# Optimization experiments

Measured on AMD Instinct MI355X. Metric: run time of the kernel, lower is better.

The kernel has to match this reference:

```python
import jax, jax.numpy as jnp
import numpy as np
from jax import lax


def conv1x1(x, w, b):
    # x: [B,C,H,W], w: [O,C], b: [O]
    return jnp.einsum('bchw,oc->bohw', x, w) + b[None, :, None, None]


def dwconv3(x, w, b):
    # depthwise 3x3, SAME padding. x: [B,C,H,W], w: [C,1,3,3], b: [C]
    C = x.shape[1]
    y = lax.conv_general_dilated(x, w, (1, 1), 'SAME',
                                 dimension_numbers=('NCHW', 'OIHW', 'NCHW'),
                                 feature_group_count=C)
    return y + b[None, :, None, None]


def proj(x, w1, b1, wd, bd):
    return dwconv3(conv1x1(x, w1, b1), wd, bd)


def setup_inputs() -> dict:
    key = jax.random.key(0)
    B, C, H, W = 8, 96, 256, 256
    ks = jax.random.split(key, 32)
    s = 0.05

    def rn(k, shape, scale=s):
        return jax.random.normal(k, shape, dtype=jnp.float32) * scale

    inp = {
        'I1': jax.random.normal(ks[0], (B, H * W, C), dtype=jnp.float32),
        'I2': jax.random.normal(ks[1], (B, H * W, C), dtype=jnp.float32),
        'h': H, 'w': W,
        'se1_w': rn(ks[2], (C, C)), 'se1_b': rn(ks[3], (C,)),
        'se1_dw': rn(ks[4], (C, 1, 3, 3)), 'se1_db': rn(ks[5], (C,)),
        'se2_w': rn(ks[6], (C, C)), 'se2_b': rn(ks[7], (C,)),
        'se2_dw': rn(ks[8], (C, 1, 3, 3)), 'se2_db': rn(ks[9], (C,)),
        'lp1_w': rn(ks[10], (C, C)), 'lp1_b': rn(ks[11], (C,)),
        'lp1_dw': rn(ks[12], (C, 1, 3, 3)), 'lp1_db': rn(ks[13], (C,)),
        'rp1_w': rn(ks[14], (C, C)), 'rp1_b': rn(ks[15], (C,)),
        'rp1_dw': rn(ks[16], (C, 1, 3, 3)), 'rp1_db': rn(ks[17], (C,)),
        'lp2_w': rn(ks[18], (C, C)), 'lp2_b': rn(ks[19], (C,)),
        'rp2_w': rn(ks[20], (C, C)), 'rp2_b': rn(ks[21], (C,)),
        'down_w': rn(ks[22], (C, 2 * C)), 'down_b': rn(ks[23], (C,)),
        'beta': rn(ks[24], (1, C, 1, 1), 0.1),
        'gamma': rn(ks[25], (1, C, 1, 1), 0.1),
    }
    return inp


def reference(I1, I2, h, w, se1_w, se1_b, se1_dw, se1_db, se2_w, se2_b,
              se2_dw, se2_db, lp1_w, lp1_b, lp1_dw, lp1_db, rp1_w, rp1_b,
              rp1_dw, rp1_db, lp2_w, lp2_b, rp2_w, rp2_b, down_w, down_b,
              beta, gamma):
    B, HW, C = I1.shape
    scale = C ** (-0.5)
    # PatchUnEmbed: [B, HW, C] -> [B, C, h, w]
    x_l = jnp.transpose(I1, (0, 2, 1)).reshape(B, C, h, w)
    x_r = jnp.transpose(I2, (0, 2, 1)).reshape(B, C, h, w)

    Q_l = jnp.transpose(proj(x_l, se1_w, se1_b, se1_dw, se1_db), (0, 2, 3, 1))  # [B,H,W,C]
    Q_r = jnp.transpose(proj(x_r, se2_w, se2_b, se2_dw, se2_db), (0, 2, 3, 1))  # [B,H,W,C]
    V_l = jnp.transpose(proj(x_l, lp1_w, lp1_b, lp1_dw, lp1_db), (0, 2, 3, 1))
    V_r = jnp.transpose(proj(x_r, rp1_w, rp1_b, rp1_dw, rp1_db), (0, 2, 3, 1))

    # row-wise cross attention along width: [B,H,W,W]
    attn = jax.nn.softmax(jnp.einsum('bhwc,bhvc->bhwv', Q_l, Q_r), axis=-1) * scale
    F_r2l = jnp.einsum('bhwv,bhvc->bhwc', attn, V_r)  # [B,H,W,C]
    F_l2r = jnp.einsum('bhwv,bhwc->bhvc', attn, V_l)  # attn^T @ V_l

    F_r2l = conv1x1(jnp.transpose(F_r2l, (0, 3, 1, 2)), lp2_w, lp2_b) * beta
    F_l2r = conv1x1(jnp.transpose(F_l2r, (0, 3, 1, 2)), rp2_w, rp2_b) * gamma

    fuse = conv1x1(jnp.concatenate([x_l + F_r2l, x_r + F_l2r], axis=1), down_w, down_b)
    # [B,C,H,W] -> [B, HW, C]
    return jnp.transpose(fuse.reshape(B, C, HW), (0, 2, 1))
```

## Files before the change

### kernel.cpp

```cpp
#include <hip/hip_runtime.h>
#include <hip/hip_bf16.h>
#include <stdint.h>

typedef __bf16 bf;
typedef __bf16 bfv8 __attribute__((ext_vector_type(8)));
typedef __bf16 bfv4 __attribute__((ext_vector_type(4)));
typedef float  f32x4 __attribute__((ext_vector_type(4)));

#define MFMA16(a,b,c) __builtin_amdgcn_mfma_f32_16x16x32_bf16((a),(b),(c),0,0,0)

#define CH  96
#define WID 256
#define HGT 256
#define NB  8
#define SCALE 0.1020620726159658f

__device__ __forceinline__ float b2f(bf x){ return (float)x; }
__device__ __forceinline__ bf   f2b(float x){ return (bf)x; }

__device__ __forceinline__ bfv8 ld_cvt8(const float* __restrict__ p){
  f32x4 a = *(const f32x4*)p;
  f32x4 b = *(const f32x4*)(p + 4);
  bfv8 r;
  r[0]=f2b(a[0]); r[1]=f2b(a[1]); r[2]=f2b(a[2]); r[3]=f2b(a[3]);
  r[4]=f2b(b[0]); r[5]=f2b(b[1]); r[6]=f2b(b[2]); r[7]=f2b(b[3]);
  return r;
}
__device__ __forceinline__ bfv4 pack4(float a,float b,float c,float d){
  bfv4 r; r[0]=f2b(a); r[1]=f2b(b); r[2]=f2b(c); r[3]=f2b(d); return r;
}

__global__ __launch_bounds__(256) void k_c1x1(
    const float* __restrict__ X,
    const float* __restrict__ Wa, const float* __restrict__ Ba,
    const float* __restrict__ Wb, const float* __restrict__ Bb,
    bf* __restrict__ Ca, bf* __restrict__ Cb)
{
  const int tid=threadIdx.x, lane=tid&63, wv=tid>>6;
  const int l15=lane&15, lg=lane>>4;
  const int set = wv&1, th = wv>>1;
  const float* W1 = set ? Wb : Wa;
  const float* B1 = set ? Bb : Ba;
  bf* C = set ? Cb : Ca;
  const size_t p0 = (size_t)blockIdx.x * 256;
  const int t0 = th*8;

  bfv8 wf[6][3];
  f32x4 bias4[6];
#pragma unroll
  for (int nt=0;nt<6;++nt){
    bias4[nt] = *(const f32x4*)(B1 + nt*16 + lg*4);
#pragma unroll
    for (int ks=0;ks<3;++ks)
      wf[nt][ks] = ld_cvt8(W1 + (nt*16+l15)*CH + ks*32 + lg*8);
  }

  bfv8 af[2][3], afn[2][3];
#pragma unroll
  for (int t=0;t<2;++t)
#pragma unroll
    for (int ks=0;ks<3;++ks)
      af[t][ks] = ld_cvt8(X + (p0 + (t0+t)*16 + l15)*CH + ks*32 + lg*8);

#pragma unroll 1
  for (int p=0;p<4;++p){
    if (p<3){
#pragma unroll
      for (int t=0;t<2;++t)
#pragma unroll
        for (int ks=0;ks<3;++ks)
          afn[t][ks] = ld_cvt8(X + (p0 + (t0+p*2+2+t)*16 + l15)*CH + ks*32 + lg*8);
    }
    f32x4 acc[2][6];
#pragma unroll
    for (int t=0;t<2;++t)
#pragma unroll
      for (int nt=0;nt<6;++nt) acc[t][nt]=bias4[nt];
#pragma unroll
    for (int ks=0;ks<3;++ks)
#pragma unroll
      for (int nt=0;nt<6;++nt)
#pragma unroll
        for (int t=0;t<2;++t)
          acc[t][nt] = MFMA16(wf[nt][ks], af[t][ks], acc[t][nt]);
#pragma unroll
    for (int t=0;t<2;++t){
      const int m0 = (t0+p*2+t)*16;
#pragma unroll
      for (int nt=0;nt<6;++nt)
        *(bfv4*)(C + (p0+m0+l15)*CH + nt*16 + lg*4)
          = pack4(acc[t][nt][0],acc[t][nt][1],acc[t][nt][2],acc[t][nt][3]);
    }
#pragma unroll
    for (int t=0;t<2;++t)
#pragma unroll
      for (int ks=0;ks<3;++ks) af[t][ks]=afn[t][ks];
  }
}

__global__ __launch_bounds__(256) void k_dw(
    const bf* __restrict__ C0, const bf* __restrict__ C1,
    const float* __restrict__ WD0, const float* __restrict__ BD0,
    const float* __restrict__ WD1, const float* __restrict__ BD1,
    bf* __restrict__ O0, bf* __restrict__ O1)
{
  const int tid = threadIdx.x;
  if (tid >= 240) return;
  const int g = tid % 12, slot = tid / 12;
  const int yrow = slot >> 2, xrun = slot & 3;
  const int b = blockIdx.z >> 1, s = blockIdx.z & 1;
  const bf* C = s ? C1 : C0;
  const float* WD = s ? WD1 : WD0;
  const float* BD = s ? BD1 : BD0;
  bf* O = s ? O1 : O0;
  const int x0 = blockIdx.x*64 + xrun*16;
  const int y  = blockIdx.y*5 + yrow;
  if (y >= HGT) return;
  const size_t ib = (size_t)b * (HGT*WID) * CH;

  float wv[9][8], bb[8];
#pragma unroll
  for (int j=0;j<8;++j){
    bb[j] = BD[g*8+j];
#pragma unroll
    for (int t=0;t<9;++t) wv[t][j] = WD[(g*8+j)*9 + t];
  }

  const bf* r0 = C + ib + ((size_t)(y-1)*WID)*CH + g*8;
  const bf* r1 = C + ib + ((size_t)(y  )*WID)*CH + g*8;
  const bf* r2 = C + ib + ((size_t)(y+1)*WID)*CH + g*8;
  const bool v0 = (y > 0), v2 = (y+1 < HGT);
  const bfv8 Z = {0,0,0,0,0,0,0,0};

  bfv8 w00,w01,w02, w10,w11,w12, w20,w21,w22;
  bfv8 na0,na1,na2, nb0,nb1,nb2;
  {
    bool vx = (x0 > 0);
    size_t o = (size_t)(x0-1)*CH;
    w00 = (v0&&vx) ? *(const bfv8*)(r0+o) : Z;
    w10 = vx       ? *(const bfv8*)(r1+o) : Z;
    w20 = (v2&&vx) ? *(const bfv8*)(r2+o) : Z;
  }
  {
    size_t o = (size_t)x0*CH;
    w01 = v0 ? *(const bfv8*)(r0+o) : Z;
    w11 =      *(const bfv8*)(r1+o);
    w21 = v2 ? *(const bfv8*)(r2+o) : Z;
  }
  {
    int xn = x0+1; bool vx = (xn < WID);
    size_t o = (size_t)xn*CH;
    na0 = (v0&&vx) ? *(const bfv8*)(r0+o) : Z;
    na1 = vx       ? *(const bfv8*)(r1+o) : Z;
    na2 = (v2&&vx) ? *(const bfv8*)(r2+o) : Z;
  }
  {
    int xn = x0+2; bool vx = (xn < WID);
    size_t o = (size_t)xn*CH;
    nb0 = (v0&&vx) ? *(const bfv8*)(r0+o) : Z;
    nb1 = vx       ? *(const bfv8*)(r1+o) : Z;
    nb2 = (v2&&vx) ? *(const bfv8*)(r2+o) : Z;
  }
#pragma unroll
  for (int xi=0; xi<16; ++xi){
    w02 = na0; w12 = na1; w22 = na2;
    na0 = nb0; na1 = nb1; na2 = nb2;
    {
      int xn = x0 + xi + 3;
      bool vx = (xn < WID) && (xi < 14);
      size_t o = (size_t)xn*CH;
      nb0 = (v0&&vx) ? *(const bfv8*)(r0+o) : Z;
      nb1 = vx       ? *(const bfv8*)(r1+o) : Z;
      nb2 = (v2&&vx) ? *(const bfv8*)(r2+o) : Z;
    }
    float acc[8];
#pragma unroll
    for (int j=0;j<8;++j) acc[j] = bb[j];
#pragma unroll
    for (int j=0;j<8;++j){
      acc[j] += wv[0][j]*b2f(w00[j]);
      acc[j] += wv[1][j]*b2f(w01[j]);
      acc[j] += wv[2][j]*b2f(w02[j]);
      acc[j] += wv[3][j]*b2f(w10[j]);
      acc[j] += wv[4][j]*b2f(w11[j]);
      acc[j] += wv[5][j]*b2f(w12[j]);
      acc[j] += wv[6][j]*b2f(w20[j]);
      acc[j] += wv[7][j]*b2f(w21[j]);
      acc[j] += wv[8][j]*b2f(w22[j]);
    }
    bfv8 st;
#pragma unroll
    for (int j=0;j<8;++j) st[j] = f2b(acc[j]);
    *(bfv8*)(O + ib + ((size_t)y*WID + x0 + xi)*CH + g*8) = st;
    w00=w01; w01=w02;
    w10=w11; w11=w12;
    w20=w21; w21=w22;
  }
}

__global__ __launch_bounds__(256) void k_attn(
    const bf* __restrict__ Ql, const bf* __restrict__ Qr,
    bf* Vl, bf* Vr)
{
  extern __shared__ char sm[];
  bf* vt = (bf*)sm;
  bf* aq = (bf*)(sm + 96*264*2);
  float* rs = (float*)(sm + 96*264*2 + 4*16*104*2);
  const int tid=threadIdx.x, lane=tid&63, wid=tid>>6;
  const int l15=lane&15, lg=lane>>4;
  bf* aqw = aq + wid*(16*104);
  const int bh = blockIdx.x;
  const size_t qoff = (size_t)bh * (WID*CH);

#pragma unroll 1
  for (int phase=0; phase<2; ++phase) {
    const bf* msrc = phase ? Qr+qoff : Ql+qoff;
    const bf* nsrc = phase ? Ql+qoff : Qr+qoff;
    bf* Vp = (phase ? Vl : Vr) + qoff;
    if (phase) {
      __syncthreads();
      rs[tid] = SCALE / rs[tid];
    }
    {
      const bfv8* src = (const bfv8*)(Vp + (size_t)tid*CH);
#pragma unroll
      for (int i=0;i<12;++i){
        bfv8 v8 = src[i];
#pragma unroll
        for (int j=0;j<8;++j) vt[(i*8+j)*264 + tid] = v8[j];
      }
    }
    __syncthreads();

#pragma unroll 1
    for (int qp=0; qp<2; ++qp){
      bfv8 af2[2][3];
#pragma unroll
      for (int q01=0;q01<2;++q01){
        const int m0 = (qp*2+q01)*64 + wid*16;
#pragma unroll
        for (int ks=0;ks<3;++ks)
          af2[q01][ks] = *(const bfv8*)(msrc + (size_t)(m0+l15)*CH + ks*32 + lg*8);
      }
      f32x4 o[2][6];
#pragma unroll
      for (int q01=0;q01<2;++q01)
#pragma unroll
        for (int nt=0;nt<6;++nt) o[q01][nt]=(f32x4){0.f,0.f,0.f,0.f};
      float rsum2[2]={0.f,0.f};

#pragma unroll 1
      for (int c4=0;c4<4;++c4){
        bfv8 nb[4][3];
#pragma unroll
        for (int nt=0;nt<4;++nt)
#pragma unroll
          for (int ks=0;ks<3;++ks)
            nb[nt][ks] = *(const bfv8*)(nsrc + (size_t)(c4*64+nt*16+l15)*CH + ks*32+lg*8);
        f32x4 fwv4[4];
        if (phase){
#pragma unroll
          for (int nt=0;nt<4;++nt)
            fwv4[nt] = *(const f32x4*)(rs + c4*64 + nt*16 + lg*4);
        }
#pragma unroll
        for (int q01=0;q01<2;++q01){
          f32x4 acc[4];
#pragma unroll
          for (int nt=0;nt<4;++nt) acc[nt]=(f32x4){0.f,0.f,0.f,0.f};
#pragma unroll
          for (int ks=0;ks<3;++ks)
#pragma unroll
            for (int nt=0;nt<4;++nt)
              acc[nt]=MFMA16(nb[nt][ks], af2[q01][ks], acc[nt]);
          if (phase==0){
#pragma unroll
            for (int nt=0;nt<4;++nt){
              float e0=__expf(acc[nt][0]), e1=__expf(acc[nt][1]);
              float e2=__expf(acc[nt][2]), e3=__expf(acc[nt][3]);
              rsum2[q01] += (e0+e1)+(e2+e3);
              *(bfv4*)(aqw + l15*104 + nt*16 + lg*4) = pack4(e0,e1,e2,e3);
            }
          } else {
#pragma unroll
            for (int nt=0;nt<4;++nt){
              float e0=__expf(acc[nt][0])*fwv4[nt][0];
              float e1=__expf(acc[nt][1])*fwv4[nt][1];
              float e2=__expf(acc[nt][2])*fwv4[nt][2];
              float e3=__expf(acc[nt][3])*fwv4[nt][3];
              *(bfv4*)(aqw + l15*104 + nt*16 + lg*4) = pack4(e0,e1,e2,e3);
            }
          }
#pragma unroll
          for (int ks=0;ks<2;++ks){
            bfv8 aa = *(const bfv8*)(aqw + l15*104 + ks*32 + lg*8);
#pragma unroll
            for (int nt=0;nt<6;++nt)
              o[q01][nt]=MFMA16(
                *(const bfv8*)(vt + (nt*16+l15)*264 + c4*64 + ks*32 + lg*8),
                aa, o[q01][nt]);
          }
        }
      }
#pragma unroll
      for (int q01=0;q01<2;++q01){
        const int m0 = (qp*2+q01)*64 + wid*16;
        float sc;
        if (phase==0){
          float rsv = rsum2[q01];
          rsv += __shfl_xor(rsv, 16, 64);
          rsv += __shfl_xor(rsv, 32, 64);
          if (lane < 16) rs[m0 + l15] = rsv;
          sc = SCALE / rsv;
        } else sc = 1.f;
#pragma unroll
        for (int nt=0;nt<6;++nt)
          *(bfv4*)(aqw + l15*104 + nt*16 + lg*4)
            = pack4(o[q01][nt][0]*sc, o[q01][nt][1]*sc,
                    o[q01][nt][2]*sc, o[q01][nt][3]*sc);
        const size_t pbase = (size_t)m0;
#pragma unroll
        for (int i=0;i<3;++i){
          int u=lane+64*i; int gr=u/12, sg=u%12;
          *(bfv8*)(Vp + (pbase+gr)*CH + sg*8)
            = *(const bfv8*)(aqw + gr*104 + sg*8);
        }
      }
    }
  }
}

__global__ __launch_bounds__(256) void k_wprep(
    const float* __restrict__ L, const float* __restrict__ lb,
    const float* __restrict__ R, const float* __restrict__ rb,
    const float* __restrict__ D, const float* __restrict__ db,
    const float* __restrict__ beta, const float* __restrict__ gamma,
    bf* __restrict__ Wcat, float* __restrict__ bv)
{
  const int o = blockIdx.x;
  const int tid = threadIdx.x;
  for (int k = tid; k < 384; k += 256){
    float v;
    if (k < 192) v = D[o*192 + k];
    else if (k < 288){
      int c = k - 192; float s = 0.f;
      for (int m=0;m<96;++m) s += D[o*192+m]*beta[m]*L[m*96+c];
      v = s;
    } else {
      int c = k - 288; float s = 0.f;
      for (int m=0;m<96;++m) s += D[o*192+96+m]*gamma[m]*R[m*96+c];
      v = s;
    }
    Wcat[o*384+k] = f2b(v);
  }
  if (tid == 0){
    float s = db[o];
    for (int m=0;m<96;++m) s += D[o*192+m]*beta[m]*lb[m] + D[o*192+96+m]*gamma[m]*rb[m];
    bv[o] = s;
  }
}

__global__ __launch_bounds__(256) void k_fuse(
    const float* __restrict__ I1, const float* __restrict__ I2,
    const bf* __restrict__ F1, const bf* __restrict__ F2,
    const bf* __restrict__ Wcat, const float* __restrict__ bv,
    float* __restrict__ OUT)
{
  const int tid=threadIdx.x, lane=tid&63, wv=tid>>6;
  const int l15=lane&15, lg=lane>>4;
  const int half = wv&1, pair = wv>>1;
  const size_t p0 = (size_t)blockIdx.x * 128;

  bfv8 wf[12][3];
  f32x4 bias4[3];
#pragma unroll
  for (int j=0;j<3;++j){
    int c = (half*3+j)*16;
    bias4[j] = *(const f32x4*)(bv + c + lg*4);
#pragma unroll
    for (int kb=0;kb<12;++kb)
      wf[kb][j] = *(const bfv8*)(Wcat + (size_t)(c+l15)*384 + kb*32 + lg*8);
  }

  bfv8 a[12], an[12];
  {
    const size_t m0 = p0 + pair*4*16;
    const float* x1 = I1 + (m0+l15)*CH + lg*8;
    const float* x2 = I2 + (m0+l15)*CH + lg*8;
    const bf* f1 = F1 + (m0+l15)*CH + lg*8;
    const bf* f2 = F2 + (m0+l15)*CH + lg*8;
#pragma unroll
    for (int ks=0;ks<3;++ks){
      a[ks]   = ld_cvt8(x1 + ks*32);
      a[3+ks] = ld_cvt8(x2 + ks*32);
      a[6+ks] = *(const bfv8*)(f1 + ks*32);
      a[9+ks] = *(const bfv8*)(f2 + ks*32);
    }
  }
#pragma unroll 1
  for (int i=0;i<4;++i){
    const size_t m0 = p0 + (pair*4+i)*16;
    if (i<3){
      const size_t mn = m0 + 16;
      const float* x1 = I1 + (mn+l15)*CH + lg*8;
      const float* x2 = I2 + (mn+l15)*CH + lg*8;
      const bf* f1 = F1 + (mn+l15)*CH + lg*8;
      const bf* f2 = F2 + (mn+l15)*CH + lg*8;
#pragma unroll
      for (int ks=0;ks<3;++ks){
        an[ks]   = ld_cvt8(x1 + ks*32);
        an[3+ks] = ld_cvt8(x2 + ks*32);
        an[6+ks] = *(const bfv8*)(f1 + ks*32);
        an[9+ks] = *(const bfv8*)(f2 + ks*32);
      }
    }
    f32x4 acc[3];
#pragma unroll
    for (int j=0;j<3;++j) acc[j]=bias4[j];
#pragma unroll
    for (int kb=0;kb<12;++kb)
#pragma unroll
      for (int j=0;j<3;++j)
        acc[j] = MFMA16(wf[kb][j], a[kb], acc[j]);
#pragma unroll
    for (int j=0;j<3;++j)
      *(f32x4*)(OUT + (m0+l15)*CH + (half*3+j)*16 + lg*4) = acc[j];
#pragma unroll
    for (int kb=0;kb<12;++kb) a[kb]=an[kb];
  }
}

extern "C" void kernel_launch(void* const* d_in, const int* in_sizes, int n_in,
                              void* d_out, int out_size, void* d_ws, size_t ws_size,
                              hipStream_t stream)
{
  (void)in_sizes; (void)n_in; (void)out_size; (void)ws_size;
  const float* I1 = (const float*)d_in[0];
  const float* I2 = (const float*)d_in[1];
  const float* se1_w = (const float*)d_in[4];
  const float* se1_b = (const float*)d_in[5];
  const float* se1_dw= (const float*)d_in[6];
  const float* se1_db= (const float*)d_in[7];
  const float* se2_w = (const float*)d_in[8];
  const float* se2_b = (const float*)d_in[9];
  const float* se2_dw= (const float*)d_in[10];
  const float* se2_db= (const float*)d_in[11];
  const float* lp1_w = (const float*)d_in[12];
  const float* lp1_b = (const float*)d_in[13];
  const float* lp1_dw= (const float*)d_in[14];
  const float* lp1_db= (const float*)d_in[15];
  const float* rp1_w = (const float*)d_in[16];
  const float* rp1_b = (const float*)d_in[17];
  const float* rp1_dw= (const float*)d_in[18];
  const float* rp1_db= (const float*)d_in[19];
  const float* lp2_w = (const float*)d_in[20];
  const float* lp2_b = (const float*)d_in[21];
  const float* rp2_w = (const float*)d_in[22];
  const float* rp2_b = (const float*)d_in[23];
  const float* down_w= (const float*)d_in[24];
  const float* down_b= (const float*)d_in[25];
  const float* beta  = (const float*)d_in[26];
  const float* gamma = (const float*)d_in[27];
  float* OUT = (float*)d_out;

  const size_t FIELD = (size_t)NB * HGT * WID * CH;
  bf* Ql = (bf*)d_ws;
  bf* Qr = Ql + FIELD;
  bf* Vl = Qr + FIELD;
  bf* Vr = Vl + FIELD;
  bf* Wcat = Vr + FIELD;
  float* bv = (float*)(Wcat + 96*384);
  bf* Cq = (bf*)d_out;
  bf* Cv = Cq + FIELD;

  dim3 blk(256,1,1);
  k_wprep<<<dim3(96,1,1), blk, 0, stream>>>(lp2_w, lp2_b, rp2_w, rp2_b,
        down_w, down_b, beta, gamma, Wcat, bv);
  k_c1x1<<<dim3(2048,1,1), blk, 0, stream>>>(I1, se1_w, se1_b, lp1_w, lp1_b, Cq, Cv);
  k_dw  <<<dim3(4,52,16),  blk, 0, stream>>>(Cq, Cv, se1_dw, se1_db, lp1_dw, lp1_db, Ql, Vl);
  k_c1x1<<<dim3(2048,1,1), blk, 0, stream>>>(I2, se2_w, se2_b, rp1_w, rp1_b, Cq, Cv);
  k_dw  <<<dim3(4,52,16),  blk, 0, stream>>>(Cq, Cv, se2_dw, se2_db, rp1_dw, rp1_db, Qr, Vr);
  k_attn<<<dim3(NB*HGT,1,1), blk, 96*264*2 + 4*16*104*2 + 256*4, stream>>>(Ql, Qr, Vl, Vr);
  k_fuse<<<dim3(4096,1,1), blk, 0, stream>>>(I1, I2, Vr, Vl, Wcat, bv, OUT);
}
```

Before: 978.3 us.

## Fuse final down-projection GEMM into attention kernel epilogue

Removes the separate k_fuse launch and runs the 1x1 fuse projection at the end of k_attn, with each block processing its own image row of 256 pixels. The intent is to save a kernel launch and to read the F_r2l/F_l2r rows while they are likely still in cache. In exchange the weights are read from global memory inside the MFMA loop instead of being held in registers, and the loads are no longer software-prefetched. Register pressure in k_attn may also rise and lower occupancy.

```diff
diff --git a/kernel.cpp b/kernel.cpp
--- a/kernel.cpp
+++ b/kernel.cpp
@@ -200,7 +200,10 @@
 
 __global__ __launch_bounds__(256) void k_attn(
     const bf* __restrict__ Ql, const bf* __restrict__ Qr,
-    bf* Vl, bf* Vr)
+    bf* Vl, bf* Vr,
+    const float* __restrict__ I1, const float* __restrict__ I2,
+    const bf* __restrict__ Wcat, const float* __restrict__ bv,
+    float* __restrict__ OUT)
 {
   extern __shared__ char sm[];
   bf* vt = (bf*)sm;
@@ -327,6 +330,47 @@
         }
       }
     }
+  }
+
+  __syncthreads();
+  const float* x1b = I1 + qoff;
+  const float* x2b = I2 + qoff;
+  const bf* f1b = Vr + qoff;
+  const bf* f2b_ = Vl + qoff;
+  float* outb = OUT + qoff;
+#pragma unroll 1
+  for (int i=0;i<4;++i){
+    const int m0 = wid*64 + i*16;
+    f32x4 acc[6];
+#pragma unroll
+    for (int nt=0;nt<6;++nt) acc[nt] = *(const f32x4*)(bv + nt*16 + lg*4);
+#pragma unroll 1
+    for (int kc=0;kc<2;++kc){
+      bfv8 a[6];
+      if (kc==0){
+#pragma unroll
+        for (int ks=0;ks<3;++ks){
+          a[ks]   = ld_cvt8(x1b + (size_t)(m0+l15)*CH + ks*32 + lg*8);
+          a[3+ks] = ld_cvt8(x2b + (size_t)(m0+l15)*CH + ks*32 + lg*8);
+        }
+      } else {
+#pragma unroll
+        for (int ks=0;ks<3;++ks){
+          a[ks]   = *(const bfv8*)(f1b  + (size_t)(m0+l15)*CH + ks*32 + lg*8);
+          a[3+ks] = *(const bfv8*)(f2b_ + (size_t)(m0+l15)*CH + ks*32 + lg*8);
+        }
+      }
+#pragma unroll
+      for (int kb=0;kb<6;++kb)
+#pragma unroll
+        for (int nt=0;nt<6;++nt)
+          acc[nt] = MFMA16(
+            *(const bfv8*)(Wcat + (size_t)(nt*16+l15)*384 + (kc*6+kb)*32 + lg*8),
+            a[kb], acc[nt]);
+    }
+#pragma unroll
+    for (int nt=0;nt<6;++nt)
+      *(f32x4*)(outb + (size_t)(m0+l15)*CH + nt*16 + lg*4) = acc[nt];
   }
 }
 
@@ -357,76 +401,6 @@
     float s = db[o];
     for (int m=0;m<96;++m) s += D[o*192+m]*beta[m]*lb[m] + D[o*192+96+m]*gamma[m]*rb[m];
     bv[o] = s;
-  }
-}
-
-__global__ __launch_bounds__(256) void k_fuse(
-    const float* __restrict__ I1, const float* __restrict__ I2,
-    const bf* __restrict__ F1, const bf* __restrict__ F2,
-    const bf* __restrict__ Wcat, const float* __restrict__ bv,
-    float* __restrict__ OUT)
-{
-  const int tid=threadIdx.x, lane=tid&63, wv=tid>>6;
-  const int l15=lane&15, lg=lane>>4;
-  const int half = wv&1, pair = wv>>1;
-  const size_t p0 = (size_t)blockIdx.x * 128;
-
-  bfv8 wf[12][3];
-  f32x4 bias4[3];
-#pragma unroll
-  for (int j=0;j<3;++j){
-    int c = (half*3+j)*16;
-    bias4[j] = *(const f32x4*)(bv + c + lg*4);
-#pragma unroll
-    for (int kb=0;kb<12;++kb)
-      wf[kb][j] = *(const bfv8*)(Wcat + (size_t)(c+l15)*384 + kb*32 + lg*8);
-  }
-
-  bfv8 a[12], an[12];
-  {
-    const size_t m0 = p0 + pair*4*16;
-    const float* x1 = I1 + (m0+l15)*CH + lg*8;
-    const float* x2 = I2 + (m0+l15)*CH + lg*8;
-    const bf* f1 = F1 + (m0+l15)*CH + lg*8;
-    const bf* f2 = F2 + (m0+l15)*CH + lg*8;
-#pragma unroll
-    for (int ks=0;ks<3;++ks){
-      a[ks]   = ld_cvt8(x1 + ks*32);
-      a[3+ks] = ld_cvt8(x2 + ks*32);
-      a[6+ks] = *(const bfv8*)(f1 + ks*32);
-      a[9+ks] = *(const bfv8*)(f2 + ks*32);
-    }
-  }
-#pragma unroll 1
-  for (int i=0;i<4;++i){
-    const size_t m0 = p0 + (pair*4+i)*16;
-    if (i<3){
-      const size_t mn = m0 + 16;
-      const float* x1 = I1 + (mn+l15)*CH + lg*8;
-      const float* x2 = I2 + (mn+l15)*CH + lg*8;
-      const bf* f1 = F1 + (mn+l15)*CH + lg*8;
-      const bf* f2 = F2 + (mn+l15)*CH + lg*8;
-#pragma unroll
-      for (int ks=0;ks<3;++ks){
-        an[ks]   = ld_cvt8(x1 + ks*32);
-        an[3+ks] = ld_cvt8(x2 + ks*32);
-        an[6+ks] = *(const bfv8*)(f1 + ks*32);
-        an[9+ks] = *(const bfv8*)(f2 + ks*32);
-      }
-    }
-    f32x4 acc[3];
-#pragma unroll
-    for (int j=0;j<3;++j) acc[j]=bias4[j];
-#pragma unroll
-    for (int kb=0;kb<12;++kb)
-#pragma unroll
-      for (int j=0;j<3;++j)
-        acc[j] = MFMA16(wf[kb][j], a[kb], acc[j]);
-#pragma unroll
-    for (int j=0;j<3;++j)
-      *(f32x4*)(OUT + (m0+l15)*CH + (half*3+j)*16 + lg*4) = acc[j];
-#pragma unroll
-    for (int kb=0;kb<12;++kb) a[kb]=an[kb];
   }
 }
 
@@ -480,6 +454,6 @@
   k_dw  <<<dim3(4,52,16),  blk, 0, stream>>>(Cq, Cv, se1_dw, se1_db, lp1_dw, lp1_db, Ql, Vl);
   k_c1x1<<<dim3(2048,1,1), blk, 0, stream>>>(I2, se2_w, se2_b, rp1_w, rp1_b, Cq, Cv);
   k_dw  <<<dim3(4,52,16),  blk, 0, stream>>>(Cq, Cv, se2_dw, se2_db, rp1_dw, rp1_db, Qr, Vr);
-  k_attn<<<dim3(NB*HGT,1,1), blk, 96*264*2 + 4*16*104*2 + 256*4, stream>>>(Ql, Qr, Vl, Vr);
-  k_fuse<<<dim3(4096,1,1), blk, 0, stream>>>(I1, I2, Vr, Vl, Wcat, bv, OUT);
-}
+  k_attn<<<dim3(NB*HGT,1,1), blk, 96*264*2 + 4*16*104*2 + 256*4, stream>>>(
+        Ql, Qr, Vl, Vr, I1, I2, Wcat, bv, OUT);
+}
```

Result: slower. 1.063 ms (+8.6%).
